# Kernel optimization log

Hardware: AMD Instinct MI355X
Metric: run time of the kernel (lower is better)

The kernel has to match this reference:

```python
import jax, jax.numpy as jnp
import numpy as np
import math

L_LAYERS = 2; B = 2; SEQ = 1024; D = 512; N = 16; H = 8; DH = 64; P = 32; KC = 4; DTR = 32

def _silu(x):
    return x * jax.nn.sigmoid(x)

def _rms(x, w, eps=1e-6):
    return x * jax.lax.rsqrt(jnp.mean(x * x, axis=-1, keepdims=True) + eps) * w

def _mamba(x, Win, conv_w, conv_b, Wx, Wdt, bdt, Alog, Dp, Wout):
    # x: [b,l,d]; mamba-ssm reference math with expand=1 (d_inner == d)
    b, l, d = x.shape
    xz = x @ Win                                   # [b,l,2d]
    xc, z = jnp.split(xz, 2, axis=-1)
    xp = jnp.pad(xc, ((0, 0), (KC - 1, 0), (0, 0)))  # causal depthwise conv
    xc = sum(xp[:, k:k + l, :] * conv_w[:, k] for k in range(KC)) + conv_b
    xc = _silu(xc)
    dbl = xc @ Wx                                  # [b,l,dtr+2N]
    dt = dbl[..., :DTR]
    Bc = dbl[..., DTR:DTR + N]                     # [b,l,N]
    Cc = dbl[..., DTR + N:]                        # [b,l,N]
    dt = jax.nn.softplus(dt @ Wdt + bdt)           # [b,l,d]
    A = -jnp.exp(Alog)                             # [d,N]
    dA = jnp.exp(dt[..., None] * A)                # [b,l,d,N]
    dBu = dt[..., None] * Bc[:, :, None, :] * xc[..., None]  # [b,l,d,N]
    def step(h, inp):
        dA_t, dBu_t, C_t = inp
        h = dA_t * h + dBu_t                       # [b,d,N]
        return h, jnp.einsum('bdn,bn->bd', h, C_t)
    h0 = jnp.zeros((b, d, N), x.dtype)
    _, ys = jax.lax.scan(step, h0, (dA.transpose(1, 0, 2, 3), dBu.transpose(1, 0, 2, 3), Cc.transpose(1, 0, 2)))
    y = ys.transpose(1, 0, 2) + Dp * xc
    y = y * _silu(z)
    return y @ Wout

def _enformer_attn(q, k, vv, u, vb, w):
    # q,k,vv: [b,l,h,d]; u,vb: [h,d]; w: [h,d,P]
    b, l, h, d = q.shape
    Pd = w.shape[-1]
    pos = jnp.arange(l)
    dist = pos[None, :] - pos[:, None]             # [l,l]
    pow_rate = jnp.exp(jnp.log((l + 1) / 2.0) / (Pd // 2))
    cw = pow_rate ** jnp.arange(1, Pd // 2 + 1, dtype=jnp.float32)
    ub = (jnp.abs(dist)[:, :, None].astype(jnp.float32) <= cw)
    sb = jnp.sign(dist)[:, :, None].astype(jnp.float32) * ub.astype(jnp.float32)
    basis = jnp.concatenate([ub.astype(jnp.float32), sb], axis=-1)  # [l,l,P]
    scale = 1.0 / math.sqrt(d)
    # qr_term without materializing r[h,l,l,d]: (q@w) then contract with basis
    qw = jnp.einsum('bihd,hdn->bhin', q, w)
    qr = jnp.einsum('bhin,ijn->bhij', qw, basis)
    uk = jnp.einsum('hd,bjhd->bhj', u, k)[:, :, None, :]
    vr = jnp.einsum('hn,ijn->hij', jnp.einsum('hd,hdn->hn', vb, w), basis)
    scores = jnp.einsum('bihd,bjhd->bhij', q, k) * scale + (qr + uk + vr[None]) * scale
    attn = jax.nn.softmax(scores, axis=-1)
    return jnp.einsum('bhij,bjhd->bihd', attn, vv)

def _forward(x, rms_m, W_in, b_in, m_Win, m_conv_w, m_conv_b, m_Wx, m_Wdt, m_bdt, m_Alog, m_D, m_Wout, W_out, b_out, rms_a, Wq, Wk, Wv, u, v, w_rel, Wo, b_o):
    b, l, dm = x.shape
    for i in range(L_LAYERS):
        # --- BidirectionalMamba block (tie_in_proj=True, tie_gate=False) ---
        skip = x
        xn = _rms(x, rms_m[i])
        proj = xn @ W_in[i] + b_in[i]              # [b,l,3*dm]
        xf = proj[..., :dm]
        zf = proj[..., dm:2 * dm]
        zr = proj[..., 2 * dm:]
        yf = _mamba(xf, m_Win[i, 0], m_conv_w[i, 0], m_conv_b[i, 0], m_Wx[i, 0], m_Wdt[i, 0], m_bdt[i, 0], m_Alog[i, 0], m_D[i, 0], m_Wout[i, 0])
        yr = jnp.flip(_mamba(jnp.flip(xf, axis=1), m_Win[i, 1], m_conv_w[i, 1], m_conv_b[i, 1], m_Wx[i, 1], m_Wdt[i, 1], m_bdt[i, 1], m_Alog[i, 1], m_D[i, 1], m_Wout[i, 1]), axis=1)
        y = yf * _silu(zf) + yr * _silu(zr)
        x = y @ W_out[i] + b_out[i] + skip
        # --- Enformer relative-position attention block ---
        skip = x
        xn = _rms(x, rms_a[i])
        q = (xn @ Wq[i]).reshape(b, l, H, DH)
        k = (xn @ Wk[i]).reshape(b, l, H, DH)
        vv = (xn @ Wv[i]).reshape(b, l, H, DH)
        o = _enformer_attn(q, k, vv, u[i], v[i], w_rel[i]).reshape(b, l, H * DH)
        x = skip + o @ Wo[i] + b_o[i]
    return x

def setup_inputs() -> dict:
    key = jax.random.key(0)
    ks = iter(jax.random.split(key, 48))
    def rn(shape, s=0.02):
        return jax.random.normal(next(ks), shape, dtype=jnp.float32) * s
    L = L_LAYERS
    inp = {}
    inp['x'] = jax.random.normal(next(ks), (B, SEQ, D), dtype=jnp.float32)
    inp['rms_m'] = jnp.ones((L, D), jnp.float32)
    inp['W_in'] = rn((L, D, 3 * D)); inp['b_in'] = jnp.zeros((L, 3 * D), jnp.float32)
    inp['m_Win'] = rn((L, 2, D, 2 * D))
    inp['m_conv_w'] = rn((L, 2, D, KC), 0.1); inp['m_conv_b'] = jnp.zeros((L, 2, D), jnp.float32)
    inp['m_Wx'] = rn((L, 2, D, DTR + 2 * N))
    inp['m_Wdt'] = rn((L, 2, DTR, D), 0.1); inp['m_bdt'] = rn((L, 2, D), 0.5)
    inp['m_Alog'] = jnp.tile(jnp.log(jnp.arange(1, N + 1, dtype=jnp.float32)), (L, 2, D, 1))
    inp['m_D'] = jnp.ones((L, 2, D), jnp.float32)
    inp['m_Wout'] = rn((L, 2, D, D))
    inp['W_out'] = rn((L, D, D)); inp['b_out'] = jnp.zeros((L, D), jnp.float32)
    inp['rms_a'] = jnp.ones((L, D), jnp.float32)
    inp['Wq'] = rn((L, D, H * DH)); inp['Wk'] = rn((L, D, H * DH)); inp['Wv'] = rn((L, D, H * DH))
    inp['u'] = rn((L, H, DH), 0.1); inp['v'] = rn((L, H, DH), 0.1)
    inp['w_rel'] = rn((L, H, DH, P), 0.1)
    inp['Wo'] = rn((L, H * DH, D)); inp['b_o'] = jnp.zeros((L, D), jnp.float32)
    return inp

def reference(x, rms_m, W_in, b_in, m_Win, m_conv_w, m_conv_b, m_Wx, m_Wdt, m_bdt, m_Alog, m_D, m_Wout, W_out, b_out, rms_a, Wq, Wk, Wv, u, v, w_rel, Wo, b_o):
    return _forward(x, rms_m, W_in, b_in, m_Win, m_conv_w, m_conv_b, m_Wx, m_Wdt, m_bdt, m_Alog, m_D, m_Wout, W_out, b_out, rms_a, Wq, Wk, Wv, u, v, w_rel, Wo, b_o)
```

## Files before the change

kernel.cpp:

```cpp
#include <hip/hip_runtime.h>

#define LL 2
#define BB 2
#define SEQL 1024
#define DD 512
#define NN 16
#define HH 8
#define DHH 64
#define PPB 32
#define KCC 4
#define DTRR 32

#define GBS 4
#define TC 64
#define NC (SEQL / TC)
#define NR (GBS * DD * NN)
#define BHN (BB * HH * SEQL)

#define AR_L     4325376L
#define OFF_WIN  0L
#define OFF_MWIN 786432L
#define OFF_WT2  1835008L
#define OFF_MWOUT 2490368L
#define OFF_WOUT 3014656L
#define OFF_QKV  3276800L
#define OFF_WO   4063232L

typedef __attribute__((ext_vector_type(8))) short bf16x8;
typedef __attribute__((ext_vector_type(4))) short short4v;
typedef __attribute__((ext_vector_type(4))) float f32x4;

__device__ __forceinline__ float siluf(float x) { return x / (1.f + __expf(-x)); }
__device__ __forceinline__ float softplusf(float x) { return x > 20.f ? x : log1pf(__expf(x)); }

__device__ __forceinline__ unsigned short f2bf(float x) {
  union { float f; unsigned u; } v; v.f = x;
  unsigned r = v.u + 0x7fff + ((v.u >> 16) & 1);
  return (unsigned short)(r >> 16);
}

__device__ __forceinline__ bf16x8 ld_frag(const unsigned short* p) {
  short4v a = *(const short4v*)(p);
  short4v b = *(const short4v*)(p + 4);
  bf16x8 r;
  r[0]=a[0]; r[1]=a[1]; r[2]=a[2]; r[3]=a[3];
  r[4]=b[0]; r[5]=b[1]; r[6]=b[2]; r[7]=b[3];
  return r;
}

__device__ __forceinline__ bf16x8 pack8(const float* p) {
  bf16x8 r;
  #pragma unroll
  for (int e = 0; e < 8; e++) r[e] = (short)f2bf(p[e]);
  return r;
}

struct TD { const float* src; unsigned short* dst; int ldsrc; int K; int N; int t0; };
struct TDs { TD a[24]; };

__global__ __launch_bounds__(256) void wtrans_all(TDs ds)
{
  int bid = blockIdx.x;
  int mi = 0;
  #pragma unroll 1
  for (int i = 1; i < 24; i++) if (bid >= ds.a[i].t0) mi = i;
  TD d = ds.a[mi];
  int local = bid - d.t0;
  int tilesN = d.N >> 5;
  int tn = local % tilesN, tk = local / tilesN;
  __shared__ float t[32][33];
  int tx = threadIdx.x & 31, ty = threadIdx.x >> 5;
  int n0 = tn * 32, k0 = tk * 32;
  #pragma unroll
  for (int i = 0; i < 4; i++)
    t[ty + 8 * i][tx] = d.src[(long)(k0 + ty + 8 * i) * d.ldsrc + n0 + tx];
  __syncthreads();
  #pragma unroll
  for (int i = 0; i < 4; i++)
    d.dst[(long)(n0 + ty + 8 * i) * d.K + k0 + tx] = f2bf(t[tx][ty + 8 * i]);
}

__global__ __launch_bounds__(256) void weff_kernel(
    const float* __restrict__ Wx, const float* __restrict__ Wdt,
    unsigned short* __restrict__ WTA)
{
  int lg = blockIdx.z;
  int l = lg >> 1, g = lg & 1;
  const float* wx = Wx + (long)(l * 2 + g) * DD * 64;
  const float* wd = Wdt + (long)(l * 2 + g) * DTRR * DD;
  unsigned short* wt = WTA + (long)l * AR_L + OFF_WT2 + (long)g * 327680;
  int n0 = blockIdx.x * 32, k0 = blockIdx.y * 32;
  __shared__ float wx_s[32][33];
  __shared__ float wd_s[32][33];
  int tx = threadIdx.x & 31, ty = threadIdx.x >> 5;
  #pragma unroll
  for (int i = 0; i < 4; i++) {
    wx_s[ty + 8 * i][tx] = wx[(long)(k0 + ty + 8 * i) * 64 + tx];
    wd_s[ty + 8 * i][tx] = wd[(long)(ty + 8 * i) * DD + n0 + tx];
  }
  __syncthreads();
  #pragma unroll
  for (int i = 0; i < 4; i++) {
    int nl = ty + 8 * i;
    float s = 0.f;
    #pragma unroll
    for (int r = 0; r < 32; r++) s = fmaf(wx_s[tx][r], wd_s[r][nl], s);
    wt[(long)(n0 + nl) * DD + k0 + tx] = f2bf(s);
  }
}

__global__ __launch_bounds__(256) void rmsinv_kernel(
    const float* __restrict__ x, float* __restrict__ inv)
{
  int row = blockIdx.x * 4 + (threadIdx.x >> 6);
  int lane = threadIdx.x & 63;
  const float* xr = x + (long)row * DD;
  float4 a = *(const float4*)(xr + lane * 4);
  float4 b = *(const float4*)(xr + 256 + lane * 4);
  float s = a.x*a.x + a.y*a.y + a.z*a.z + a.w*a.w + b.x*b.x + b.y*b.y + b.z*b.z + b.w*b.w;
  for (int o = 32; o; o >>= 1) s += __shfl_down(s, o);
  if (lane == 0) inv[row] = rsqrtf(s / (float)DD + 1e-6f);
}

template<int BM, int BN>
__global__ __launch_bounds__(256) void gemm_bf16_t(
    const float* __restrict__ A, const unsigned short* __restrict__ WT,
    const float* __restrict__ bias, const float* __restrict__ resid,
    const float* __restrict__ invrow, const float* __restrict__ colw,
    float* __restrict__ C,
    int M, int N, int K, int lda, int ldc,
    long aBatch, long wBatch, long biasBatch, long cBatch,
    int aflipL, int act)
{
  constexpr int FM = BM / 32;
  constexpr int FN = BN / 32;
  int g = blockIdx.z;
  A  += (long)g * aBatch;
  WT += (long)g * wBatch;
  C  += (long)g * cBatch;
  if (bias) bias += (long)g * biasBatch;
  const bool flip = (aflipL > 0) && (g == 1);

  __shared__ unsigned short A_lds[BM][72];
  __shared__ unsigned short B_lds[BN][72];
  int tid = threadIdx.x;
  int w = tid >> 6, lane = tid & 63, li = lane & 15, lg = lane >> 4;
  int bm = blockIdx.y * BM, bn = blockIdx.x * BN;
  int wm = (w & 1) * (BM / 2), wn = (w >> 1) * (BN / 2);
  f32x4 acc[FM][FN] = {};

  const int kqA = (tid & 15) * 4, r0A = tid >> 4;
  const int kqB = (tid & 7) * 8,  r0B = tid >> 3;

  for (int k0 = 0; k0 < K; k0 += 64) {
    __syncthreads();
    float4 cw4 = {1.f, 1.f, 1.f, 1.f};
    if (colw) cw4 = *(const float4*)(colw + k0 + kqA);
    #pragma unroll
    for (int i = 0; i < BM / 16; i++) {
      int m = bm + r0A + 16 * i;
      int mm = m;
      if (flip) { int bb = m / aflipL; int t = m - bb * aflipL; mm = bb * aflipL + (aflipL - 1 - t); }
      float4 av = *(const float4*)(A + (long)mm * lda + k0 + kqA);
      float sc = invrow ? invrow[mm] : 1.f;
      short4v ap = { (short)f2bf(av.x * sc * cw4.x), (short)f2bf(av.y * sc * cw4.y),
                     (short)f2bf(av.z * sc * cw4.z), (short)f2bf(av.w * sc * cw4.w) };
      *(short4v*)(&A_lds[r0A + 16 * i][kqA]) = ap;
    }
    #pragma unroll
    for (int i = 0; i < BN / 32; i++) {
      int n = bn + r0B + 32 * i;
      bf16x8 bv = *(const bf16x8*)(WT + (long)n * K + k0 + kqB);
      *(bf16x8*)(&B_lds[r0B + 32 * i][kqB]) = bv;
    }
    __syncthreads();
    #pragma unroll
    for (int ks = 0; ks < 2; ks++) {
      bf16x8 af[FM], bfr[FN];
      #pragma unroll
      for (int fm = 0; fm < FM; fm++)
        af[fm] = *(const bf16x8*)(&A_lds[wm + fm * 16 + li][ks * 32 + lg * 8]);
      #pragma unroll
      for (int fn = 0; fn < FN; fn++)
        bfr[fn] = *(const bf16x8*)(&B_lds[wn + fn * 16 + li][ks * 32 + lg * 8]);
      #pragma unroll
      for (int fm = 0; fm < FM; fm++)
        #pragma unroll
        for (int fn = 0; fn < FN; fn++)
          acc[fm][fn] = __builtin_amdgcn_mfma_f32_16x16x32_bf16(af[fm], bfr[fn], acc[fm][fn], 0, 0, 0);
    }
  }
  #pragma unroll
  for (int fm = 0; fm < FM; fm++) {
    #pragma unroll
    for (int fn = 0; fn < FN; fn++) {
      int n = bn + wn + fn * 16 + li;
      float bv = bias ? bias[n] : 0.f;
      #pragma unroll
      for (int r = 0; r < 4; r++) {
        int m = bm + wm + fm * 16 + 4 * lg + r;
        float v = acc[fm][fn][r] + bv;
        if (act == 1) v = softplusf(v);
        if (resid) v += resid[(long)m * ldc + n];
        C[(long)m * ldc + n] = v;
      }
    }
  }
}

__global__ __launch_bounds__(256) void gemm_dtbc(
    const float* __restrict__ A, const unsigned short* __restrict__ WT2,
    const float* __restrict__ bdt, float* __restrict__ dtv, float* __restrict__ bc,
    int layer)
{
  int g = blockIdx.z;
  A   += (long)g * BB * SEQL * DD;
  WT2 += (long)g * 640 * DD;
  dtv += (long)g * BB * SEQL * DD;
  bc  += (long)g * BB * SEQL * 32;
  bdt += (long)(layer * 2 + g) * DD;

  __shared__ unsigned short A_lds[64][72];
  __shared__ unsigned short B_lds[64][72];
  int tid = threadIdx.x;
  int w = tid >> 6, lane = tid & 63, li = lane & 15, lg = lane >> 4;
  int bm = blockIdx.y * 64, bn = blockIdx.x * 64;
  int wm = (w & 1) * 32, wn = (w >> 1) * 32;
  f32x4 acc[2][2] = {};

  const int kqA = (tid & 15) * 4, r0A = tid >> 4;
  const int kqB = (tid & 7) * 8,  r0B = tid >> 3;

  for (int k0 = 0; k0 < DD; k0 += 64) {
    __syncthreads();
    #pragma unroll
    for (int i = 0; i < 4; i++) {
      int m = bm + r0A + 16 * i;
      float4 av = *(const float4*)(A + (long)m * DD + k0 + kqA);
      short4v ap = { (short)f2bf(av.x), (short)f2bf(av.y), (short)f2bf(av.z), (short)f2bf(av.w) };
      *(short4v*)(&A_lds[r0A + 16 * i][kqA]) = ap;
    }
    #pragma unroll
    for (int i = 0; i < 2; i++) {
      int n = bn + r0B + 32 * i;
      bf16x8 bv = *(const bf16x8*)(WT2 + (long)n * DD + k0 + kqB);
      *(bf16x8*)(&B_lds[r0B + 32 * i][kqB]) = bv;
    }
    __syncthreads();
    #pragma unroll
    for (int ks = 0; ks < 2; ks++) {
      bf16x8 af[2], bfr[2];
      #pragma unroll
      for (int fm = 0; fm < 2; fm++)
        af[fm] = *(const bf16x8*)(&A_lds[wm + fm * 16 + li][ks * 32 + lg * 8]);
      #pragma unroll
      for (int fn = 0; fn < 2; fn++)
        bfr[fn] = *(const bf16x8*)(&B_lds[wn + fn * 16 + li][ks * 32 + lg * 8]);
      #pragma unroll
      for (int fm = 0; fm < 2; fm++)
        #pragma unroll
        for (int fn = 0; fn < 2; fn++)
          acc[fm][fn] = __builtin_amdgcn_mfma_f32_16x16x32_bf16(af[fm], bfr[fn], acc[fm][fn], 0, 0, 0);
    }
  }
  #pragma unroll
  for (int fm = 0; fm < 2; fm++) {
    #pragma unroll
    for (int fn = 0; fn < 2; fn++) {
      int n = bn + wn + fn * 16 + li;
      if (n < 512) {
        float bv = bdt[n];
        #pragma unroll
        for (int r = 0; r < 4; r++) {
          int m = bm + wm + fm * 16 + 4 * lg + r;
          dtv[(long)m * DD + n] = softplusf(acc[fm][fn][r] + bv);
        }
      } else if (n < 544) {
        #pragma unroll
        for (int r = 0; r < 4; r++) {
          int m = bm + wm + fm * 16 + 4 * lg + r;
          bc[(long)m * 32 + (n - 512)] = acc[fm][fn][r];
        }
      }
    }
  }
}

__global__ __launch_bounds__(256) void conv_silu_kernel(
    const float* __restrict__ xz, const float* __restrict__ cw, const float* __restrict__ cb,
    float* __restrict__ xc, int layer)
{
  long idx = (long)blockIdx.x * 256 + threadIdx.x;
  int c = idx % DD;
  long r = idx / DD;
  int t = r % SEQL;
  long gb = r / SEQL;
  int g = (int)(gb / BB);
  const float* w = cw + ((long)(layer * 2 + g) * DD + c) * KCC;
  float acc = cb[(long)(layer * 2 + g) * DD + c];
  const float* xp = xz + (r - t) * 2 * DD + c;
  #pragma unroll
  for (int k = 0; k < KCC; k++) {
    int tt = t - (KCC - 1) + k;
    if (tt >= 0) acc = fmaf(xp[(long)tt * 2 * DD], w[k], acc);
  }
  xc[idx] = siluf(acc);
}

__global__ __launch_bounds__(256) void scan_chunk_kernel(
    const float* __restrict__ dtv, const float* __restrict__ xc,
    const float* __restrict__ bc, const float* __restrict__ Alog,
    float* __restrict__ P, float* __restrict__ Hend, int layer)
{
  int chunk = blockIdx.x, dtile = blockIdx.y, gb = blockIdx.z;
  int g = gb / BB;
  int tid = threadIdx.x;
  int n = tid & 15, dl = tid >> 4;
  int d = dtile * 16 + dl;
  int t0 = chunk * TC;
  __shared__ float dtv_s[TC][16], xc_s[TC][16], B_s[TC][17];
  {
    int c = tid & 15, rr = tid >> 4;
    long base = ((long)gb * SEQL + t0) * DD + dtile * 16;
    long dbase = ((long)gb * SEQL + t0) * 32;
    #pragma unroll
    for (int i = 0; i < 4; i++) {
      int tl = rr + i * 16;
      dtv_s[tl][c] = dtv[base + (long)tl * DD + c];
      xc_s[tl][c]  = xc[base + (long)tl * DD + c];
      B_s[tl][c]   = bc[dbase + (long)tl * 32 + c];
    }
  }
  __syncthreads();
  float a = -__expf(Alog[((long)((layer * 2 + g) * DD) + d) * NN + n]);
  float h = 0.f, sdt = 0.f;
  #pragma unroll 4
  for (int t = 0; t < TC; t++) {
    float dt = dtv_s[t][dl];
    float dA = __expf(dt * a);
    h = fmaf(dA, h, dt * B_s[t][n] * xc_s[t][dl]);
    sdt += dt;
  }
  int r = (gb * DD + d) * NN + n;
  long o = (long)chunk * NR + r;
  P[o] = __expf(a * sdt);
  Hend[o] = h;
}

__global__ __launch_bounds__(256) void scan_combine_kernel(
    const float* __restrict__ P, const float* __restrict__ Hend, float* __restrict__ Hin)
{
  int r = blockIdx.x * 256 + threadIdx.x;
  float h = 0.f;
  #pragma unroll
  for (int c = 0; c < NC; c++) {
    Hin[(long)c * NR + r] = h;
    h = fmaf(P[(long)c * NR + r], h, Hend[(long)c * NR + r]);
  }
}

__global__ __launch_bounds__(256) void scan_apply_kernel(
    const float* __restrict__ dtv, const float* __restrict__ xc, const float* __restrict__ xz,
    const float* __restrict__ bc, const float* __restrict__ Alog, const float* __restrict__ Dp,
    const float* __restrict__ Hin, float* __restrict__ ym, int layer)
{
  int chunk = blockIdx.x, dtile = blockIdx.y, gb = blockIdx.z;
  int g = gb / BB;
  int tid = threadIdx.x;
  int n = tid & 15, dl = tid >> 4;
  int d = dtile * 16 + dl;
  int t0 = chunk * TC;
  __shared__ float dtv_s[TC][16], xc_s[TC][16], B_s[TC][17], C_s[TC][17], y_s[TC][16];
  {
    int c = tid & 15, rr = tid >> 4;
    long base = ((long)gb * SEQL + t0) * DD + dtile * 16;
    long dbase = ((long)gb * SEQL + t0) * 32;
    #pragma unroll
    for (int i = 0; i < 4; i++) {
      int tl = rr + i * 16;
      dtv_s[tl][c] = dtv[base + (long)tl * DD + c];
      xc_s[tl][c]  = xc[base + (long)tl * DD + c];
      B_s[tl][c]   = bc[dbase + (long)tl * 32 + c];
      C_s[tl][c]   = bc[dbase + (long)tl * 32 + 16 + c];
    }
  }
  __syncthreads();
  float a = -__expf(Alog[((long)((layer * 2 + g) * DD) + d) * NN + n]);
  int r = (gb * DD + d) * NN + n;
  float h = Hin[(long)chunk * NR + r];
  #pragma unroll 4
  for (int t = 0; t < TC; t++) {
    float dt = dtv_s[t][dl];
    float dA = __expf(dt * a);
    h = fmaf(dA, h, dt * B_s[t][n] * xc_s[t][dl]);
    float val = h * C_s[t][n];
    val += __shfl_xor(val, 1);
    val += __shfl_xor(val, 2);
    val += __shfl_xor(val, 4);
    val += __shfl_xor(val, 8);
    if (n == 0) y_s[t][dl] = val;
  }
  __syncthreads();
  {
    int c = tid & 15, rr = tid >> 4;
    long base = ((long)gb * SEQL + t0) * DD + dtile * 16;
    long zbase = ((long)gb * SEQL + t0) * 2 * DD + DD + dtile * 16;
    float Dpc = Dp[(long)(layer * 2 + g) * DD + dtile * 16 + c];
    #pragma unroll
    for (int i = 0; i < 4; i++) {
      int tl = rr + i * 16;
      float z = xz[zbase + (long)tl * 2 * DD + c];
      ym[base + (long)tl * DD + c] = (y_s[tl][c] + Dpc * xc_s[tl][c]) * siluf(z);
    }
  }
}

__global__ __launch_bounds__(256) void combine_kernel(
    const float* __restrict__ yp, const float* __restrict__ proj, float* __restrict__ yc)
{
  long idx = (long)blockIdx.x * 256 + threadIdx.x;
  int d = idx % DD;
  long r = idx / DD;
  int t = r % SEQL;
  long b = r / SEQL;
  float y0 = yp[idx];
  float y1 = yp[(long)BB * SEQL * DD + (b * SEQL + (SEQL - 1 - t)) * (long)DD + d];
  const float* pr = proj + r * 3 * DD;
  float zf = pr[DD + d];
  float zr = pr[2 * DD + d];
  yc[idx] = y0 * siluf(zf) + y1 * siluf(zr);
}

__global__ void tab_kernel(unsigned short* __restrict__ tab)
{
  int idx = blockIdx.x * blockDim.x + threadIdx.x;
  if (idx >= 2047) return;
  int di = idx - 1023;
  int ad = di < 0 ? -di : di;
  float pr = expf(logf((SEQL + 1) * 0.5f) / 16.0f);
  int n0 = 16;
  for (int n = 15; n >= 0; n--) {
    float cw = powf(pr, (float)(n + 1));
    if ((float)ad <= cw) n0 = n;
  }
  tab[idx] = (unsigned short)(di == 0 ? 34 : (di < 0 ? n0 : 17 + n0));
}

__global__ __launch_bounds__(256) void qw_kernel(
    const float* __restrict__ q, const float* __restrict__ w_rel, float* __restrict__ S, int layer)
{
  int itile = blockIdx.x;
  int bh = blockIdx.y;
  int h = bh % HH, b = bh / HH;
  int i0 = itile * 64;
  __shared__ float q_s[64][65];
  __shared__ float w_s[64][33];
  __shared__ float qwn[64][33];
  int tid = threadIdx.x;
  {
    int r = tid >> 2, c4 = (tid & 3) * 16;
    const float* qr = q + ((long)(b * SEQL + i0 + r)) * DD + h * 64 + c4;
    #pragma unroll
    for (int e = 0; e < 4; e++) {
      float4 v = *(const float4*)(qr + e * 4);
      q_s[r][c4 + e * 4 + 0] = v.x; q_s[r][c4 + e * 4 + 1] = v.y;
      q_s[r][c4 + e * 4 + 2] = v.z; q_s[r][c4 + e * 4 + 3] = v.w;
    }
  }
  for (int idx = tid; idx < 64 * 32; idx += 256) {
    int d = idx >> 5, n = idx & 31;
    w_s[d][n] = w_rel[((long)(layer * HH + h) * DHH + d) * PPB + n];
  }
  __syncthreads();
  {
    int i = tid & 63, ngrp = tid >> 6;
    float acc[8] = {};
    #pragma unroll 8
    for (int d = 0; d < 64; d++) {
      float qv = q_s[i][d];
      #pragma unroll
      for (int e = 0; e < 8; e++) acc[e] = fmaf(qv, w_s[d][ngrp * 8 + e], acc[e]);
    }
    #pragma unroll
    for (int e = 0; e < 8; e++) qwn[i][ngrp * 8 + e] = acc[e];
  }
  __syncthreads();
  for (int idx = tid; idx < 64 * 17; idx += 256) {
    int il = idx / 17, m = idx % 17;
    float s1 = 0.f, s2 = 0.f;
    for (int n = m; n < 16; n++) { s1 += qwn[il][n]; s2 += qwn[il][16 + n]; }
    float* Sp = S + ((long)bh * SEQL + i0 + il) * 34;
    Sp[m] = s1;
    Sp[17 + m] = s2;
  }
}

__global__ __launch_bounds__(256) void vw_kernel(
    const float* __restrict__ vparam, const float* __restrict__ w_rel, float* __restrict__ VS)
{
  int layer = blockIdx.x;
  __shared__ float vws[HH][PPB];
  int tid = threadIdx.x;
  int h = tid / PPB, n = tid % PPB;
  const float* vp = vparam + (long)(layer * HH + h) * DHH;
  const float* wp = w_rel + ((long)(layer * HH + h) * DHH) * PPB + n;
  float s = 0.f;
  for (int d = 0; d < DHH; d++) s = fmaf(vp[d], wp[d * PPB], s);
  vws[h][n] = s;
  __syncthreads();
  if (tid < HH * 17) {
    int hh = tid / 17, m = tid % 17;
    float s1 = 0.f, s2 = 0.f;
    for (int nn = m; nn < 16; nn++) { s1 += vws[hh][nn]; s2 += vws[hh][16 + nn]; }
    VS[layer * 272 + hh * 34 + m] = s1;
    VS[layer * 272 + hh * 34 + 17 + m] = s2;
  }
}

__global__ __launch_bounds__(256) void uk_kernel(
    const float* __restrict__ u, const float* __restrict__ k, float* __restrict__ uk, int layer)
{
  int wid = (blockIdx.x * 256 + threadIdx.x) >> 6;
  int lane = threadIdx.x & 63;
  if (wid >= BB * HH * SEQL) return;
  int j = wid % SEQL;
  int bh = wid / SEQL;
  int h = bh % HH;
  int b = bh / HH;
  float vv = u[(long)(layer * HH + h) * DHH + lane] * k[((long)(b * SEQL + j) * HH + h) * DHH + lane];
  for (int o = 32; o; o >>= 1) vv += __shfl_down(vv, o);
  if (lane == 0) uk[(long)bh * SEQL + j] = vv;
}

__global__ __launch_bounds__(256) void attn_mfma_kernel(
    const float* __restrict__ q, const float* __restrict__ k, const float* __restrict__ vv,
    const float* __restrict__ S, const float* __restrict__ VS, const float* __restrict__ uk,
    const unsigned short* __restrict__ tab,
    float* __restrict__ opart, float* __restrict__ mbuf, float* __restrict__ lbuf)
{
  __shared__ __align__(16) char smem[39680];
  unsigned short* K_lds  = (unsigned short*)(smem);
  unsigned short* VT_lds = (unsigned short*)(smem + 8704);
  unsigned short* PT_lds = (unsigned short*)(smem + 17408);
  float* E               = (float*)(smem + 26112);
  unsigned short* tab_s  = (unsigned short*)(smem + 35328);
  float* uk_s            = (float*)(smem + 39424);
  float* O_lds           = (float*)(smem);

  int itile = blockIdx.x;
  int bh = blockIdx.y;
  int split = blockIdx.z;
  int h = bh % HH, b = bh / HH;
  int i0 = itile * 64;
  int tid = threadIdx.x;
  int w = tid >> 6;
  int lane = tid & 63;
  int li = lane & 15, lg = lane >> 4;

  for (int idx = tid; idx < 64 * 17; idx += 256) {
    int il = idx / 17, m = idx % 17;
    long srow = ((long)bh * SEQL + i0 + il) * 34;
    float c0 = S[srow + m]      + VS[h * 34 + m];
    float c1 = S[srow + 17 + m] + VS[h * 34 + 17 + m];
    E[il * 36 + m]      = c0 - c1;
    E[il * 36 + 17 + m] = c0 + c1;
    if (m == 0) E[il * 36 + 34] = c0;
  }
  for (int idx = tid; idx < 2047; idx += 256) tab_s[idx] = tab[idx];

  int iq = i0 + w * 16 + li;
  const float* qrow = q + ((long)(b * SEQL + iq)) * DD + h * 64;
  bf16x8 qf0 = pack8(qrow + 8 * lg);
  bf16x8 qf1 = pack8(qrow + 32 + 8 * lg);

  f32x4 oacc[4] = {};
  float mrun = -1e30f, lrun = 0.f;
  const int ibase = i0 + w * 16 + li;
  unsigned short* PTw = PT_lds + w * 16 * 68;
  const float* Erow = E + (w * 16 + li) * 36;

  const int jbase = split * (SEQL / 2);
  for (int jt = 0; jt < SEQL / 2; jt += 64) {
    int j0 = jbase + jt;
    __syncthreads();
    {
      int jl = tid >> 4;
      int dq = (tid & 15) * 4;
      #pragma unroll
      for (int rr = 0; rr < 4; rr++) {
        int jj = jl + rr * 16;
        long grow = ((long)(b * SEQL + j0 + jj)) * DD + h * 64 + dq;
        float4 kv = *(const float4*)(k + grow);
        short4v kp = { (short)f2bf(kv.x), (short)f2bf(kv.y), (short)f2bf(kv.z), (short)f2bf(kv.w) };
        *(short4v*)(K_lds + jj * 68 + dq) = kp;
        float4 vvv = *(const float4*)(vv + grow);
        VT_lds[(dq + 0) * 68 + jj] = f2bf(vvv.x);
        VT_lds[(dq + 1) * 68 + jj] = f2bf(vvv.y);
        VT_lds[(dq + 2) * 68 + jj] = f2bf(vvv.z);
        VT_lds[(dq + 3) * 68 + jj] = f2bf(vvv.w);
      }
      if (tid < 64) uk_s[tid] = uk[(long)bh * SEQL + j0 + tid];
    }
    __syncthreads();

    f32x4 sf[4];
    #pragma unroll
    for (int jj = 0; jj < 4; jj++) {
      f32x4 c = {};
      c = __builtin_amdgcn_mfma_f32_16x16x32_bf16(
            ld_frag(K_lds + (jj * 16 + li) * 68 + 8 * lg), qf0, c, 0, 0, 0);
      c = __builtin_amdgcn_mfma_f32_16x16x32_bf16(
            ld_frag(K_lds + (jj * 16 + li) * 68 + 32 + 8 * lg), qf1, c, 0, 0, 0);
      sf[jj] = c;
    }

    float sv[4][4];
    float tmax = -1e30f;
    #pragma unroll
    for (int jj = 0; jj < 4; jj++) {
      #pragma unroll
      for (int r = 0; r < 4; r++) {
        int jloc = jj * 16 + 4 * lg + r;
        int di = (j0 + jloc) - ibase;
        int id = tab_s[1023 + di];
        float val = (sf[jj][r] + Erow[id] + uk_s[jloc]) * 0.125f;
        sv[jj][r] = val;
        tmax = fmaxf(tmax, val);
      }
    }
    tmax = fmaxf(tmax, __shfl_xor(tmax, 16));
    tmax = fmaxf(tmax, __shfl_xor(tmax, 32));
    float mnew = fmaxf(mrun, tmax);
    float fsc = __expf(mrun - mnew);
    mrun = mnew;
    lrun *= fsc;
    #pragma unroll
    for (int df = 0; df < 4; df++) oacc[df] *= fsc;

    float psum = 0.f;
    #pragma unroll
    for (int jj = 0; jj < 4; jj++) {
      short4v pk;
      #pragma unroll
      for (int r = 0; r < 4; r++) {
        float p = __expf(sv[jj][r] - mnew);
        psum += p;
        pk[r] = (short)f2bf(p);
      }
      *(short4v*)(PTw + li * 68 + jj * 16 + 4 * lg) = pk;
    }
    psum += __shfl_xor(psum, 16);
    psum += __shfl_xor(psum, 32);
    lrun += psum;

    asm volatile("s_waitcnt lgkmcnt(0)" ::: "memory");

    bf16x8 pf0 = ld_frag(PTw + li * 68 + 8 * lg);
    bf16x8 pf1 = ld_frag(PTw + li * 68 + 32 + 8 * lg);
    #pragma unroll
    for (int df = 0; df < 4; df++) {
      f32x4 c = oacc[df];
      c = __builtin_amdgcn_mfma_f32_16x16x32_bf16(
            ld_frag(VT_lds + (df * 16 + li) * 68 + 8 * lg), pf0, c, 0, 0, 0);
      c = __builtin_amdgcn_mfma_f32_16x16x32_bf16(
            ld_frag(VT_lds + (df * 16 + li) * 68 + 32 + 8 * lg), pf1, c, 0, 0, 0);
      oacc[df] = c;
    }
  }

  __syncthreads();
  if (lg == 0) {
    long row = (long)split * BHN + (long)bh * SEQL + (i0 + w * 16 + li);
    mbuf[row] = mrun;
    lbuf[row] = lrun;
  }
  #pragma unroll
  for (int df = 0; df < 4; df++)
    *(f32x4*)(O_lds + (w * 16 + li) * 68 + df * 16 + 4 * lg) = oacc[df];
  __syncthreads();
  {
    int il = tid >> 2, c0 = (tid & 3) * 16;
    long orow = ((long)split * BHN + (long)bh * SEQL + i0 + il) * 64 + c0;
    #pragma unroll
    for (int c4 = 0; c4 < 4; c4++) {
      f32x4 o = *(const f32x4*)(O_lds + il * 68 + c0 + c4 * 4);
      *(f32x4*)(opart + orow + c4 * 4) = o;
    }
  }
}

__global__ __launch_bounds__(256) void attn_combine_kernel(
    const float* __restrict__ opart, const float* __restrict__ mbuf,
    const float* __restrict__ lbuf, float* __restrict__ out)
{
  int idx = blockIdx.x * 256 + threadIdx.x;
  int row = idx >> 6, d = idx & 63;
  int bh = row >> 10, i = row & 1023;
  int b = bh >> 3, h = bh & 7;
  float m0 = mbuf[row], m1 = mbuf[BHN + row];
  float l0 = lbuf[row], l1 = lbuf[BHN + row];
  float m = fmaxf(m0, m1);
  float e0 = __expf(m0 - m), e1 = __expf(m1 - m);
  float inv = 1.f / (l0 * e0 + l1 * e1);
  float o = (opart[(long)row * 64 + d] * e0 + opart[((long)BHN + row) * 64 + d] * e1) * inv;
  out[((long)(b * SEQL + i)) * DD + h * 64 + d] = o;
}

extern "C" void kernel_launch(void* const* d_in, const int* in_sizes, int n_in,
                              void* d_out, int out_size, void* d_ws, size_t ws_size,
                              hipStream_t stream) {
  const float* x_in     = (const float*)d_in[0];
  const float* rms_m    = (const float*)d_in[1];
  const float* W_in     = (const float*)d_in[2];
  const float* b_in     = (const float*)d_in[3];
  const float* m_Win    = (const float*)d_in[4];
  const float* m_conv_w = (const float*)d_in[5];
  const float* m_conv_b = (const float*)d_in[6];
  const float* m_Wx     = (const float*)d_in[7];
  const float* m_Wdt    = (const float*)d_in[8];
  const float* m_bdt    = (const float*)d_in[9];
  const float* m_Alog   = (const float*)d_in[10];
  const float* m_Dp     = (const float*)d_in[11];
  const float* m_Wout   = (const float*)d_in[12];
  const float* W_out    = (const float*)d_in[13];
  const float* b_out    = (const float*)d_in[14];
  const float* rms_a    = (const float*)d_in[15];
  const float* Wq       = (const float*)d_in[16];
  const float* Wk       = (const float*)d_in[17];
  const float* Wv       = (const float*)d_in[18];
  const float* u_p      = (const float*)d_in[19];
  const float* v_p      = (const float*)d_in[20];
  const float* w_rel    = (const float*)d_in[21];
  const float* Wo       = (const float*)d_in[22];
  const float* b_o      = (const float*)d_in[23];
  float* out = (float*)d_out;

  float* ws = (float*)d_ws;
  const long U = (long)BB * SEQL * DD;
  float* xA    = ws;
  float* xB    = ws + 1 * U;
  float* xn    = ws + 2 * U;
  float* proj  = ws + 3 * U;
  float* xz    = ws + 6 * U;
  float* xc    = ws + 10 * U;
  float* dtv   = ws + 12 * U;
  float* ym    = ws + 14 * U;
  float* ycomb = ws + 16 * U;
  float* smallb= ws + 17 * U;
  float* bcbuf = smallb;
  float* ukbuf = smallb + 262144;
  float* Sbuf  = smallb + 278528;
  float* VSbuf = smallb + 835584;
  unsigned short* tabg = (unsigned short*)(smallb + 836880);
  float* invm  = smallb + 838928;
  float* inva  = smallb + 840976;
  unsigned short* WTA = (unsigned short*)(ws + 18 * U);
  float* yp = xz;
  float* qb = proj;
  float* kb = proj + U;
  float* vb = proj + 2 * U;
  float* attnout = ym;
  float* Pbuf = xn;
  float* Hend = xn + (long)NC * NR;
  float* Hin  = ycomb;
  float* opart = xc;
  float* mbuf  = dtv;
  float* lbuf  = dtv + 2 * BHN;

  const int M = BB * SEQL;

  tab_kernel<<<8, 256, 0, stream>>>(tabg);

  TDs td;
  int cum = 0, idx = 0;
  auto add = [&](const float* s, unsigned short* dst, int ldsrc, int K, int N) {
    td.a[idx].src = s; td.a[idx].dst = dst; td.a[idx].ldsrc = ldsrc;
    td.a[idx].K = K; td.a[idx].N = N; td.a[idx].t0 = cum;
    cum += (N / 32) * (K / 32); idx++;
  };
  for (int l = 0; l < LL; l++) {
    unsigned short* base = WTA + (long)l * AR_L;
    add(W_in   + (long)l * DD * 3 * DD,        base + OFF_WIN,            3 * DD, DD, 3 * DD);
    add(m_Win  + (long)(l * 2 + 0) * DD * 2 * DD, base + OFF_MWIN,          2 * DD, DD, 2 * DD);
    add(m_Win  + (long)(l * 2 + 1) * DD * 2 * DD, base + OFF_MWIN + 524288, 2 * DD, DD, 2 * DD);
    add(m_Wout + (long)(l * 2 + 0) * DD * DD,  base + OFF_MWOUT,          DD, DD, DD);
    add(m_Wout + (long)(l * 2 + 1) * DD * DD,  base + OFF_MWOUT + 262144, DD, DD, DD);
    add(W_out  + (long)l * DD * DD,            base + OFF_WOUT,           DD, DD, DD);
    add(Wq     + (long)l * DD * DD,            base + OFF_QKV,            DD, DD, DD);
    add(Wk     + (long)l * DD * DD,            base + OFF_QKV + 262144,   DD, DD, DD);
    add(Wv     + (long)l * DD * DD,            base + OFF_QKV + 524288,   DD, DD, DD);
    add(Wo     + (long)l * DD * DD,            base + OFF_WO,             DD, DD, DD);
    add(m_Wx   + (long)(l * 2 + 0) * DD * 64 + 32, base + OFF_WT2 + 262144,          64, DD, 32);
    add(m_Wx   + (long)(l * 2 + 1) * DD * 64 + 32, base + OFF_WT2 + 327680 + 262144, 64, DD, 32);
  }
  wtrans_all<<<cum, 256, 0, stream>>>(td);
  weff_kernel<<<dim3(16, 16, 2 * LL), 256, 0, stream>>>(m_Wx, m_Wdt, WTA);
  vw_kernel<<<LL, 256, 0, stream>>>(v_p, w_rel, VSbuf);

  for (int layer = 0; layer < LL; layer++) {
    const float* cur = (layer == 0) ? x_in : xA;
    unsigned short* base = WTA + (long)layer * AR_L;
    rmsinv_kernel<<<M / 4, 256, 0, stream>>>(cur, invm);
    gemm_bf16_t<64, 64><<<dim3(24, 32, 1), 256, 0, stream>>>(cur, base + OFF_WIN,
        b_in + layer * 3 * DD, nullptr, invm, rms_m + layer * DD, proj,
        M, 3 * DD, DD, DD, 3 * DD, 0, 0, 0, 0, 0, 0);
    gemm_bf16_t<64, 64><<<dim3(16, 32, 2), 256, 0, stream>>>(proj, base + OFF_MWIN,
        nullptr, nullptr, nullptr, nullptr, xz, M, 2 * DD, DD, 3 * DD, 2 * DD,
        0, 524288, 0, (long)BB * SEQL * 2 * DD, SEQL, 0);
    conv_silu_kernel<<<(2 * BB * SEQL * DD) / 256, 256, 0, stream>>>(xz, m_conv_w, m_conv_b, xc, layer);
    gemm_dtbc<<<dim3(9, 32, 2), 256, 0, stream>>>(xc, base + OFF_WT2, m_bdt, dtv, bcbuf, layer);
    scan_chunk_kernel<<<dim3(NC, DD / 16, GBS), 256, 0, stream>>>(
        dtv, xc, bcbuf, m_Alog, Pbuf, Hend, layer);
    scan_combine_kernel<<<NR / 256, 256, 0, stream>>>(Pbuf, Hend, Hin);
    scan_apply_kernel<<<dim3(NC, DD / 16, GBS), 256, 0, stream>>>(
        dtv, xc, xz, bcbuf, m_Alog, m_Dp, Hin, ym, layer);
    gemm_bf16_t<64, 64><<<dim3(8, 32, 2), 256, 0, stream>>>(ym, base + OFF_MWOUT,
        nullptr, nullptr, nullptr, nullptr, yp, M, DD, DD, DD, DD,
        U, 262144, 0, U, 0, 0);
    combine_kernel<<<(int)(U / 256), 256, 0, stream>>>(yp, proj, ycomb);
    gemm_bf16_t<64, 64><<<dim3(8, 32, 1), 256, 0, stream>>>(ycomb, base + OFF_WOUT,
        b_out + layer * DD, cur, nullptr, nullptr, xB, M, DD, DD, DD, DD, 0, 0, 0, 0, 0, 0);

    rmsinv_kernel<<<M / 4, 256, 0, stream>>>(xB, inva);
    gemm_bf16_t<64, 64><<<dim3(8, 32, 3), 256, 0, stream>>>(xB, base + OFF_QKV,
        nullptr, nullptr, inva, rms_a + layer * DD, qb, M, DD, DD, DD, DD,
        0, 262144, 0, U, 0, 0);
    qw_kernel<<<dim3(16, 16), 256, 0, stream>>>(qb, w_rel, Sbuf, layer);
    uk_kernel<<<(BB * HH * SEQL) / 4, 256, 0, stream>>>(u_p, kb, ukbuf, layer);
    attn_mfma_kernel<<<dim3(SEQL / 64, BB * HH, 2), 256, 0, stream>>>(
        qb, kb, vb, Sbuf, VSbuf + layer * 272, ukbuf, tabg, opart, mbuf, lbuf);
    attn_combine_kernel<<<(BHN * 64) / 256, 256, 0, stream>>>(opart, mbuf, lbuf, attnout);

    float* outp = (layer == LL - 1) ? out : xA;
    gemm_bf16_t<64, 64><<<dim3(8, 32, 1), 256, 0, stream>>>(attnout, base + OFF_WO,
        b_o + layer * DD, xB, nullptr, nullptr, outp, M, DD, DD, DD, DD, 0, 0, 0, 0, 0, 0);
  }
}
```

Baseline: 614.5 us.

## Restructure selective scan so each thread carries eight states with vectorized tiles

The chunked scan kernels now give each thread 8 of the 16 state elements for one channel, and each block covers 128 channels instead of 16. Global-to-shared loads and the output epilogue use float4, B and C are read from shared memory as float4, and the per-timestep reduction across lanes drops from four shuffles to one. The chunk length is halved to 32, which doubles the number of chunks and the work in the sequential combine pass but shortens each serial chunk scan. Hend is moved to the xB buffer because the larger P/Hend arrays no longer fit in xn.

```diff
diff --git a/kernel.cpp b/kernel.cpp
--- a/kernel.cpp
+++ b/kernel.cpp
@@ -12,7 +12,7 @@
 #define DTRR 32
 
 #define GBS 4
-#define TC 64
+#define TC 32
 #define NC (SEQL / TC)
 #define NR (GBS * DD * NN)
 #define BHN (BB * HH * SEQL)
@@ -315,36 +315,50 @@
   int chunk = blockIdx.x, dtile = blockIdx.y, gb = blockIdx.z;
   int g = gb / BB;
   int tid = threadIdx.x;
-  int n = tid & 15, dl = tid >> 4;
-  int d = dtile * 16 + dl;
+  int dl = tid >> 1, nh = (tid & 1) * 8;
+  int d = dtile * 128 + dl;
   int t0 = chunk * TC;
-  __shared__ float dtv_s[TC][16], xc_s[TC][16], B_s[TC][17];
+  __shared__ float dtv_s[TC][128], xc_s[TC][128], BC_s[TC][32];
   {
-    int c = tid & 15, rr = tid >> 4;
-    long base = ((long)gb * SEQL + t0) * DD + dtile * 16;
+    long base = ((long)gb * SEQL + t0) * DD + dtile * 128;
+    int c4 = (tid & 31) * 4, r0 = tid >> 5;
+    #pragma unroll
+    for (int i = 0; i < 4; i++) {
+      int tl = r0 + i * 8;
+      *(float4*)&dtv_s[tl][c4] = *(const float4*)(dtv + base + (long)tl * DD + c4);
+      *(float4*)&xc_s[tl][c4]  = *(const float4*)(xc + base + (long)tl * DD + c4);
+    }
     long dbase = ((long)gb * SEQL + t0) * 32;
-    #pragma unroll
-    for (int i = 0; i < 4; i++) {
-      int tl = rr + i * 16;
-      dtv_s[tl][c] = dtv[base + (long)tl * DD + c];
-      xc_s[tl][c]  = xc[base + (long)tl * DD + c];
-      B_s[tl][c]   = bc[dbase + (long)tl * 32 + c];
-    }
-  }
-  __syncthreads();
-  float a = -__expf(Alog[((long)((layer * 2 + g) * DD) + d) * NN + n]);
-  float h = 0.f, sdt = 0.f;
-  #pragma unroll 4
+    int cc = (tid & 7) * 4, rr = tid >> 3;
+    *(float4*)&BC_s[rr][cc] = *(const float4*)(bc + dbase + (long)rr * 32 + cc);
+  }
+  __syncthreads();
+  const float* Al = Alog + ((long)((layer * 2 + g) * DD) + d) * NN + nh;
+  float a[8], h[8] = {};
+  #pragma unroll
+  for (int n = 0; n < 8; n++) a[n] = -__expf(Al[n]);
+  float sdt = 0.f;
   for (int t = 0; t < TC; t++) {
     float dt = dtv_s[t][dl];
-    float dA = __expf(dt * a);
-    h = fmaf(dA, h, dt * B_s[t][n] * xc_s[t][dl]);
+    float dx = dt * xc_s[t][dl];
+    float4 b0 = *(const float4*)&BC_s[t][nh];
+    float4 b1 = *(const float4*)&BC_s[t][nh + 4];
+    h[0] = fmaf(__expf(dt * a[0]), h[0], dx * b0.x);
+    h[1] = fmaf(__expf(dt * a[1]), h[1], dx * b0.y);
+    h[2] = fmaf(__expf(dt * a[2]), h[2], dx * b0.z);
+    h[3] = fmaf(__expf(dt * a[3]), h[3], dx * b0.w);
+    h[4] = fmaf(__expf(dt * a[4]), h[4], dx * b1.x);
+    h[5] = fmaf(__expf(dt * a[5]), h[5], dx * b1.y);
+    h[6] = fmaf(__expf(dt * a[6]), h[6], dx * b1.z);
+    h[7] = fmaf(__expf(dt * a[7]), h[7], dx * b1.w);
     sdt += dt;
   }
-  int r = (gb * DD + d) * NN + n;
-  long o = (long)chunk * NR + r;
-  P[o] = __expf(a * sdt);
-  Hend[o] = h;
+  long o = (long)chunk * NR + ((long)(gb * DD + d)) * NN + nh;
+  #pragma unroll
+  for (int n = 0; n < 8; n++) {
+    P[o + n] = __expf(a[n] * sdt);
+    Hend[o + n] = h[n];
+  }
 }
 
 __global__ __launch_bounds__(256) void scan_combine_kernel(
@@ -367,50 +381,76 @@
   int chunk = blockIdx.x, dtile = blockIdx.y, gb = blockIdx.z;
   int g = gb / BB;
   int tid = threadIdx.x;
-  int n = tid & 15, dl = tid >> 4;
-  int d = dtile * 16 + dl;
+  int dl = tid >> 1, nh = (tid & 1) * 8;
+  int d = dtile * 128 + dl;
   int t0 = chunk * TC;
-  __shared__ float dtv_s[TC][16], xc_s[TC][16], B_s[TC][17], C_s[TC][17], y_s[TC][16];
+  __shared__ float dtv_s[TC][128], xc_s[TC][128], BC_s[TC][32], y_s[TC][128];
   {
-    int c = tid & 15, rr = tid >> 4;
-    long base = ((long)gb * SEQL + t0) * DD + dtile * 16;
+    long base = ((long)gb * SEQL + t0) * DD + dtile * 128;
+    int c4 = (tid & 31) * 4, r0 = tid >> 5;
+    #pragma unroll
+    for (int i = 0; i < 4; i++) {
+      int tl = r0 + i * 8;
+      *(float4*)&dtv_s[tl][c4] = *(const float4*)(dtv + base + (long)tl * DD + c4);
+      *(float4*)&xc_s[tl][c4]  = *(const float4*)(xc + base + (long)tl * DD + c4);
+    }
     long dbase = ((long)gb * SEQL + t0) * 32;
-    #pragma unroll
-    for (int i = 0; i < 4; i++) {
-      int tl = rr + i * 16;
-      dtv_s[tl][c] = dtv[base + (long)tl * DD + c];
-      xc_s[tl][c]  = xc[base + (long)tl * DD + c];
-      B_s[tl][c]   = bc[dbase + (long)tl * 32 + c];
-      C_s[tl][c]   = bc[dbase + (long)tl * 32 + 16 + c];
-    }
-  }
-  __syncthreads();
-  float a = -__expf(Alog[((long)((layer * 2 + g) * DD) + d) * NN + n]);
-  int r = (gb * DD + d) * NN + n;
-  float h = Hin[(long)chunk * NR + r];
-  #pragma unroll 4
+    int cc = (tid & 7) * 4, rr = tid >> 3;
+    *(float4*)&BC_s[rr][cc] = *(const float4*)(bc + dbase + (long)rr * 32 + cc);
+  }
+  __syncthreads();
+  const float* Al = Alog + ((long)((layer * 2 + g) * DD) + d) * NN + nh;
+  float a[8], h[8];
+  #pragma unroll
+  for (int n = 0; n < 8; n++) a[n] = -__expf(Al[n]);
+  {
+    long r = (long)chunk * NR + ((long)(gb * DD + d)) * NN + nh;
+    float4 h0 = *(const float4*)(Hin + r);
+    float4 h1 = *(const float4*)(Hin + r + 4);
+    h[0]=h0.x; h[1]=h0.y; h[2]=h0.z; h[3]=h0.w;
+    h[4]=h1.x; h[5]=h1.y; h[6]=h1.z; h[7]=h1.w;
+  }
   for (int t = 0; t < TC; t++) {
     float dt = dtv_s[t][dl];
-    float dA = __expf(dt * a);
-    h = fmaf(dA, h, dt * B_s[t][n] * xc_s[t][dl]);
-    float val = h * C_s[t][n];
+    float dx = dt * xc_s[t][dl];
+    float4 b0 = *(const float4*)&BC_s[t][nh];
+    float4 b1 = *(const float4*)&BC_s[t][nh + 4];
+    float4 c0 = *(const float4*)&BC_s[t][16 + nh];
+    float4 c1 = *(const float4*)&BC_s[t][16 + nh + 4];
+    h[0] = fmaf(__expf(dt * a[0]), h[0], dx * b0.x);
+    h[1] = fmaf(__expf(dt * a[1]), h[1], dx * b0.y);
+    h[2] = fmaf(__expf(dt * a[2]), h[2], dx * b0.z);
+    h[3] = fmaf(__expf(dt * a[3]), h[3], dx * b0.w);
+    h[4] = fmaf(__expf(dt * a[4]), h[4], dx * b1.x);
+    h[5] = fmaf(__expf(dt * a[5]), h[5], dx * b1.y);
+    h[6] = fmaf(__expf(dt * a[6]), h[6], dx * b1.z);
+    h[7] = fmaf(__expf(dt * a[7]), h[7], dx * b1.w);
+    float v0 = h[0] * c0.x + h[1] * c0.y;
+    float v1 = h[2] * c0.z + h[3] * c0.w;
+    float v2 = h[4] * c1.x + h[5] * c1.y;
+    float v3 = h[6] * c1.z + h[7] * c1.w;
+    float val = (v0 + v1) + (v2 + v3);
     val += __shfl_xor(val, 1);
-    val += __shfl_xor(val, 2);
-    val += __shfl_xor(val, 4);
-    val += __shfl_xor(val, 8);
-    if (n == 0) y_s[t][dl] = val;
+    if ((tid & 1) == 0) y_s[t][dl] = val;
   }
   __syncthreads();
   {
-    int c = tid & 15, rr = tid >> 4;
-    long base = ((long)gb * SEQL + t0) * DD + dtile * 16;
-    long zbase = ((long)gb * SEQL + t0) * 2 * DD + DD + dtile * 16;
-    float Dpc = Dp[(long)(layer * 2 + g) * DD + dtile * 16 + c];
+    long base = ((long)gb * SEQL + t0) * DD + dtile * 128;
+    long zbase = ((long)gb * SEQL + t0) * 2 * DD + DD + dtile * 128;
+    int c4 = (tid & 31) * 4, r0 = tid >> 5;
+    float4 Dp4 = *(const float4*)(Dp + (long)(layer * 2 + g) * DD + dtile * 128 + c4);
     #pragma unroll
     for (int i = 0; i < 4; i++) {
-      int tl = rr + i * 16;
-      float z = xz[zbase + (long)tl * 2 * DD + c];
-      ym[base + (long)tl * DD + c] = (y_s[tl][c] + Dpc * xc_s[tl][c]) * siluf(z);
+      int tl = r0 + i * 8;
+      float4 y4 = *(const float4*)&y_s[tl][c4];
+      float4 x4 = *(const float4*)&xc_s[tl][c4];
+      float4 z4 = *(const float4*)(xz + zbase + (long)tl * 2 * DD + c4);
+      float4 o;
+      o.x = (y4.x + Dp4.x * x4.x) * siluf(z4.x);
+      o.y = (y4.y + Dp4.y * x4.y) * siluf(z4.y);
+      o.z = (y4.z + Dp4.z * x4.z) * siluf(z4.z);
+      o.w = (y4.w + Dp4.w * x4.w) * siluf(z4.w);
+      *(float4*)(ym + base + (long)tl * DD + c4) = o;
     }
   }
 }
@@ -761,7 +801,7 @@
   float* vb = proj + 2 * U;
   float* attnout = ym;
   float* Pbuf = xn;
-  float* Hend = xn + (long)NC * NR;
+  float* Hend = xB;
   float* Hin  = ycomb;
   float* opart = xc;
   float* mbuf  = dtv;
@@ -809,10 +849,10 @@
         0, 524288, 0, (long)BB * SEQL * 2 * DD, SEQL, 0);
     conv_silu_kernel<<<(2 * BB * SEQL * DD) / 256, 256, 0, stream>>>(xz, m_conv_w, m_conv_b, xc, layer);
     gemm_dtbc<<<dim3(9, 32, 2), 256, 0, stream>>>(xc, base + OFF_WT2, m_bdt, dtv, bcbuf, layer);
-    scan_chunk_kernel<<<dim3(NC, DD / 16, GBS), 256, 0, stream>>>(
+    scan_chunk_kernel<<<dim3(NC, DD / 128, GBS), 256, 0, stream>>>(
         dtv, xc, bcbuf, m_Alog, Pbuf, Hend, layer);
     scan_combine_kernel<<<NR / 256, 256, 0, stream>>>(Pbuf, Hend, Hin);
-    scan_apply_kernel<<<dim3(NC, DD / 16, GBS), 256, 0, stream>>>(
+    scan_apply_kernel<<<dim3(NC, DD / 128, GBS), 256, 0, stream>>>(
         dtv, xc, xz, bcbuf, m_Alog, m_Dp, Hin, ym, layer);
     gemm_bf16_t<64, 64><<<dim3(8, 32, 2), 256, 0, stream>>>(ym, base + OFF_MWOUT,
         nullptr, nullptr, nullptr, nullptr, yp, M, DD, DD, DD, DD,
```

After: 575.9 us. -6.3%, faster.
